# Optimization experiments

Measured on AMD Instinct MI355X. Metric: run time of the kernel, lower is better.

Reference implementation:

```python
import jax, jax.numpy as jnp
import numpy as np

IN_CHANNELS = 64
OUT_CHANNELS = 64

def setup_inputs() -> dict:
    key = jax.random.key(0)
    k1, k2 = jax.random.split(key)
    shape = (8, IN_CHANNELS, 256, 256)
    x_real = jax.random.normal(k1, shape, dtype=jnp.float32)
    x_imag = jax.random.normal(k2, shape, dtype=jnp.float32)
    return {"x_real": x_real, "x_imag": x_imag}

def reference(x_real, x_imag):
    # weight is all-ones [Cout, Cin, 1, 1]: the 1x1 conv is a sum over input
    # channels broadcast to every output channel.
    # real/imag channel-sums: [B, 1, H, W]
    r = jnp.sum(x_real, axis=1, keepdims=True)
    i = jnp.sum(x_imag, axis=1, keepdims=True)
    # broadcast to out_channels and pack complex: [B, Cout, H, W]
    out = jax.lax.complex(
        jnp.broadcast_to(r, (x_real.shape[0], OUT_CHANNELS) + x_real.shape[2:]),
        jnp.broadcast_to(i, (x_imag.shape[0], OUT_CHANNELS) + x_imag.shape[2:]),
    )
    return out
```

## Files before the change

kernel.cpp:

```cpp
#include <hip/hip_runtime.h>


#define CHANNELS 64
#define HW (256 * 256)
#define HW4 (HW / 4)

typedef float f4 __attribute__((ext_vector_type(4)));

__global__ __launch_bounds__(256)
void identity_conv_real_kernel(const f4* __restrict__ xr,
                               f4* __restrict__ out,
                               int total) {
    int gid = blockIdx.x * blockDim.x + threadIdx.x;
    if (gid >= total) return;

    int b  = gid >> 14;
    int p4 = gid & (HW4 - 1);

    const f4* xr_b = xr + (size_t)b * CHANNELS * HW4 + p4;

    f4 r = (f4)(0.f);
    #pragma unroll 16
    for (int c = 0; c < CHANNELS; ++c) {
        r += xr_b[(size_t)c * HW4];
    }

    f4* ob = out + (size_t)b * CHANNELS * HW4 + p4;
    #pragma unroll 16
    for (int co = 0; co < CHANNELS; ++co) {
        __builtin_nontemporal_store(r, &ob[(size_t)co * HW4]);
    }
}

__global__ __launch_bounds__(256)
void identity_conv_cplx_kernel(const f4* __restrict__ xr,
                               const f4* __restrict__ xi,
                               f4* __restrict__ out,
                               int total) {
    int gid = blockIdx.x * blockDim.x + threadIdx.x;
    if (gid >= total) return;

    int b  = gid >> 14;
    int p4 = gid & (HW4 - 1);

    const f4* xr_b = xr + (size_t)b * CHANNELS * HW4 + p4;
    const f4* xi_b = xi + (size_t)b * CHANNELS * HW4 + p4;

    f4 r  = (f4)(0.f);
    f4 im = (f4)(0.f);
    #pragma unroll 8
    for (int c = 0; c < CHANNELS; ++c) {
        r  += xr_b[(size_t)c * HW4];
        im += xi_b[(size_t)c * HW4];
    }

    f4 lo = (f4){r.x, im.x, r.y, im.y};
    f4 hi = (f4){r.z, im.z, r.w, im.w};

    f4* ob = out + (size_t)b * CHANNELS * (HW / 2) + (size_t)p4 * 2;
    #pragma unroll 4
    for (int co = 0; co < CHANNELS; ++co) {
        __builtin_nontemporal_store(lo, &ob[0]);
        __builtin_nontemporal_store(hi, &ob[1]);
        ob += HW / 2;
    }
}

extern "C" void kernel_launch(void* const* d_in, const int* in_sizes, int n_in,
                              void* d_out, int out_size, void* d_ws, size_t ws_size,
                              hipStream_t stream) {
    const f4* xr = (const f4*)d_in[0];
    const f4* xi = (const f4*)d_in[1];
    f4* out = (f4*)d_out;

    int n = in_sizes[0];
    int B = n / (CHANNELS * HW);
    int total = B * HW4;

    const int block = 256;
    int grid = (total + block - 1) / block;

    if (out_size >= 2 * n) {
        identity_conv_cplx_kernel<<<grid, block, 0, stream>>>(xr, xi, out, total);
    } else {
        identity_conv_real_kernel<<<grid, block, 0, stream>>>(xr, out, total);
    }
}
```

Before: 47.92 us.

## Split real-path into channel-sum and grid-stride broadcast kernels, drop nontemporal stores

Measured after the change: 47.76 us. No clear change (-0.3%).

```diff
diff --git a/kernel.cpp b/kernel.cpp
--- a/kernel.cpp
+++ b/kernel.cpp
@@ -4,13 +4,45 @@
 #define CHANNELS 64
 #define HW (256 * 256)
 #define HW4 (HW / 4)
+#define OUT_SHIFT 20
 
 typedef float f4 __attribute__((ext_vector_type(4)));
 
 __global__ __launch_bounds__(256)
-void identity_conv_real_kernel(const f4* __restrict__ xr,
-                               f4* __restrict__ out,
-                               int total) {
+void channel_sum_kernel(const f4* __restrict__ xr,
+                        f4* __restrict__ r,
+                        int total) {
+    int gid = blockIdx.x * blockDim.x + threadIdx.x;
+    if (gid >= total) return;
+
+    int b  = gid >> 14;
+    int p4 = gid & (HW4 - 1);
+
+    const f4* base = xr + (size_t)b * CHANNELS * HW4 + p4;
+    f4 s = (f4)(0.f);
+    #pragma unroll 16
+    for (int c = 0; c < CHANNELS; ++c)
+        s += base[(size_t)c * HW4];
+
+    r[gid] = s;
+}
+
+__global__ __launch_bounds__(256)
+void broadcast_kernel(const f4* __restrict__ r,
+                      f4* __restrict__ out,
+                      int total_out) {
+    int stride = gridDim.x * blockDim.x;
+    for (int i = blockIdx.x * blockDim.x + threadIdx.x; i < total_out; i += stride) {
+        int b  = i >> OUT_SHIFT;
+        int p4 = i & (HW4 - 1);
+        out[i] = r[(b << 14) + p4];
+    }
+}
+
+__global__ __launch_bounds__(256)
+void identity_conv_fused_kernel(const f4* __restrict__ xr,
+                                f4* __restrict__ out,
+                                int total) {
     int gid = blockIdx.x * blockDim.x + threadIdx.x;
     if (gid >= total) return;
 
@@ -18,18 +50,15 @@
     int p4 = gid & (HW4 - 1);
 
     const f4* xr_b = xr + (size_t)b * CHANNELS * HW4 + p4;
-
-    f4 r = (f4)(0.f);
+    f4 s = (f4)(0.f);
     #pragma unroll 16
-    for (int c = 0; c < CHANNELS; ++c) {
-        r += xr_b[(size_t)c * HW4];
-    }
+    for (int c = 0; c < CHANNELS; ++c)
+        s += xr_b[(size_t)c * HW4];
 
     f4* ob = out + (size_t)b * CHANNELS * HW4 + p4;
     #pragma unroll 16
-    for (int co = 0; co < CHANNELS; ++co) {
-        __builtin_nontemporal_store(r, &ob[(size_t)co * HW4]);
-    }
+    for (int co = 0; co < CHANNELS; ++co)
+        ob[(size_t)co * HW4] = s;
 }
 
 __global__ __launch_bounds__(256)
@@ -60,8 +89,8 @@
     f4* ob = out + (size_t)b * CHANNELS * (HW / 2) + (size_t)p4 * 2;
     #pragma unroll 4
     for (int co = 0; co < CHANNELS; ++co) {
-        __builtin_nontemporal_store(lo, &ob[0]);
-        __builtin_nontemporal_store(hi, &ob[1]);
+        ob[0] = lo;
+        ob[1] = hi;
         ob += HW / 2;
     }
 }
@@ -75,14 +104,27 @@
 
     int n = in_sizes[0];
     int B = n / (CHANNELS * HW);
-    int total = B * HW4;
+    int total_r = B * HW4;
 
     const int block = 256;
-    int grid = (total + block - 1) / block;
 
     if (out_size >= 2 * n) {
-        identity_conv_cplx_kernel<<<grid, block, 0, stream>>>(xr, xi, out, total);
+        int grid = (total_r + block - 1) / block;
+        identity_conv_cplx_kernel<<<grid, block, 0, stream>>>(xr, xi, out, total_r);
+        return;
+    }
+
+    size_t ws_needed = (size_t)total_r * sizeof(f4);
+    if (ws_size >= ws_needed) {
+        f4* r = (f4*)d_ws;
+        int grid1 = (total_r + block - 1) / block;
+        channel_sum_kernel<<<grid1, block, 0, stream>>>(xr, r, total_r);
+
+        int total_out = out_size / 4;
+        int grid2 = 2048;
+        broadcast_kernel<<<grid2, block, 0, stream>>>(r, out, total_out);
     } else {
-        identity_conv_real_kernel<<<grid, block, 0, stream>>>(xr, out, total);
+        int grid = (total_r + block - 1) / block;
+        identity_conv_fused_kernel<<<grid, block, 0, stream>>>(xr, out, total_r);
     }
 }
```
